# Kernel tuning notes

Measured on AMD Instinct MI355X. Metric: run time of the kernel, lower is better.

## Reference

```python
import jax, jax.numpy as jnp
import numpy as np

B, C, H, W = 4, 256, 128, 128
WS = 16                      # window_size
DA = 64                      # dim_attn = dim // head_dim_reduce_ratio
MID = 1024                   # mid_dim = dim * ratio
SCALE = DA ** -0.5           # num_heads=1 -> dim_head = DA


def setup_inputs() -> dict:
    key = jax.random.key(0)
    ks = jax.random.split(key, 14)
    def w(k, shape, std=0.02):
        return jax.random.normal(k, shape, dtype=jnp.float32) * std
    return {
        "x": jax.random.normal(ks[0], (B, C, H, W), dtype=jnp.float32),
        "q_w": w(ks[1], (DA, C)),
        "q_s": jax.random.uniform(ks[2], (DA,), minval=0.5, maxval=1.5),
        "q_b": w(ks[3], (DA,), 0.1),
        "k_w": w(ks[4], (DA, C)),
        "k_s": jax.random.uniform(ks[5], (DA,), minval=0.5, maxval=1.5),
        "k_b": w(ks[6], (DA,), 0.1),
        "vg_w": w(ks[7], (2 * MID, C)),
        "vg_s": jax.random.uniform(ks[8], (2 * MID,), minval=0.5, maxval=1.5),
        "vg_b": w(ks[9], (2 * MID,), 0.1),
        "p_w": w(ks[10], (C, MID)),
        "p_s": jax.random.uniform(ks[11], (C,), minval=0.5, maxval=1.5),
        "p_b": w(ks[12], (C,), 0.1),
    }


def _conv1x1_bn(xf, w, s, b):
    # xf: [Bw, Cin, N]; 1x1 conv + folded BatchNorm (per-channel affine)
    return jnp.einsum("oc,bcn->bon", w, xf) * s[:, None] + b[:, None]


def reference(x, q_w, q_s, q_b, k_w, k_s, k_b, vg_w, vg_s, vg_b, p_w, p_s, p_b):
    nH, nW = H // WS, W // WS
    # window_partition: [B,C,H,W] -> [B*nH*nW, C, WS, WS]
    xw = x.reshape(B, C, nH, WS, nW, WS).transpose(0, 2, 4, 1, 3, 5)
    xf = xw.reshape(B * nH * nW, C, WS * WS)  # [Bw, C, N]

    # v_gate conv -> sigmoid applied to BOTH halves (matches source)
    vg = jax.nn.sigmoid(_conv1x1_bn(xf, vg_w, vg_s, vg_b))   # [Bw, 2*MID, N]
    v, gate = jnp.split(vg, 2, axis=1)                        # [Bw, MID, N] each

    q = _conv1x1_bn(xf, q_w, q_s, q_b) * SCALE                # [Bw, DA, N]
    k = _conv1x1_bn(xf, k_w, k_s, k_b)                        # [Bw, DA, N]

    attn = jax.nn.softmax(jnp.einsum("bcn,bcm->bnm", q, k), axis=-1)  # [Bw, N, N]
    out = jnp.einsum("bcm,bnm->bcn", v, attn)                 # v @ attn^T -> [Bw, MID, N]
    out = out * gate
    out = _conv1x1_bn(out, p_w, p_s, p_b)                     # [Bw, C, N]

    # window_reverse: [B*nH*nW, C, WS, WS] -> [B, C, H, W]
    out = out.reshape(B, nH, nW, C, WS, WS).transpose(0, 3, 1, 4, 2, 5)
    return out.reshape(B, C, H, W)
```

## Files before the change

### kernel.cpp

```cpp
#include <hip/hip_runtime.h>
#include <hip/hip_bf16.h>

#define B_    4
#define C_    256
#define H_    128
#define W_    128
#define NW_   256
#define N_    256
#define DA_   64
#define MID_  1024
#define SCALE_ 0.125f

typedef __attribute__((ext_vector_type(8))) __bf16 frag8;
typedef __attribute__((ext_vector_type(4))) float  f32x4;
typedef __attribute__((ext_vector_type(4))) unsigned int u32x4;

#define MFMA(a, b, c) __builtin_amdgcn_mfma_f32_16x16x32_bf16(a, b, c, 0, 0, 0)

__device__ __forceinline__ unsigned short f2bf(float x) {
    union { float f; unsigned u; } v; v.f = x;
    unsigned r = v.u + 0x7FFFu + ((v.u >> 16) & 1u);
    return (unsigned short)(r >> 16);
}
__device__ __forceinline__ float bf2f(unsigned short h) {
    union { unsigned u; float f; } v; v.u = ((unsigned)h) << 16;
    return v.f;
}
__device__ __forceinline__ frag8 loadf8(const unsigned short* p) {
    return *reinterpret_cast<const frag8*>(p);
}

__global__ void k_wprep(const float* __restrict__ qw, const float* __restrict__ qs,
                        const float* __restrict__ kw, const float* __restrict__ ks,
                        const float* __restrict__ vgw, const float* __restrict__ vgs,
                        const float* __restrict__ pw, const float* __restrict__ ps,
                        unsigned short* __restrict__ wvg,
                        unsigned short* __restrict__ wqk,
                        unsigned short* __restrict__ wp) {
    int i = blockIdx.x * 256 + threadIdx.x;
    if (i < 2048 * 256) {
        int r = i >> 8;
        wvg[i] = f2bf(vgw[i] * vgs[r]);
        return;
    }
    int j = i - 2048 * 256;
    if (j < 128 * 256) {
        int r = j >> 8, c = j & 255;
        float v = (r < 64) ? qw[r * 256 + c] * qs[r] * SCALE_
                           : kw[(r - 64) * 256 + c] * ks[r - 64];
        wqk[j] = f2bf(v);
        return;
    }
    int m = j - 128 * 256;
    if (m < 256 * 1024) {
        int o = m >> 10;
        wp[m] = f2bf(pw[m] * ps[o]);
    }
}

__global__ void k_pack(const float* __restrict__ x, unsigned short* __restrict__ xfT) {
    __shared__ unsigned short tile[64][258];
    int wdw = blockIdx.x >> 2, cq = blockIdx.x & 3;
    int b = wdw >> 6, wh = (wdw >> 3) & 7, ww = wdw & 7;
    int tid = threadIdx.x;
    int n = tid;
    int h = wh * 16 + (n >> 4), wc = ww * 16 + (n & 15);
    const float* xb = x + ((long)(b * C_ + cq * 64)) * (H_ * W_) + h * W_ + wc;
    #pragma unroll 4
    for (int cl = 0; cl < 64; ++cl)
        tile[cl][n] = f2bf(xb[cl * H_ * W_]);
    __syncthreads();
    unsigned short* dst = xfT + (long)wdw * (N_ * C_) + cq * 64;
    int cl = tid & 63;
    #pragma unroll 4
    for (int it = 0; it < 64; ++it) {
        int nn = it * 4 + (tid >> 6);
        dst[nn * C_ + cl] = tile[cl][nn];
    }
}

__global__ __launch_bounds__(512) void k_attn(const unsigned short* __restrict__ xfT,
                                              const unsigned short* __restrict__ wqk,
                                              const float* __restrict__ qb,
                                              const float* __restrict__ kb,
                                              unsigned short* __restrict__ attn) {
    __shared__ __align__(16) unsigned short qT[256][72];
    __shared__ __align__(16) unsigned short kT[256][72];
    __shared__ __align__(16) char wqlds[65536];
    int wdw = blockIdx.x;
    int tid = threadIdx.x, w = tid >> 6, l = tid & 63;
    int l16 = l & 15, lg = l >> 4;
    const unsigned short* xw = xfT + (long)wdw * (N_ * C_);

    {
        int srow = tid >> 2;
        int cb = (tid & 3) * 128;
        const u32x4* src = reinterpret_cast<const u32x4*>(wqk + srow * 256 + (tid & 3) * 64);
        int sw = (srow & 7) << 4;
        #pragma unroll
        for (int j = 0; j < 8; ++j)
            *reinterpret_cast<u32x4*>(wqlds + srow * 512 + ((cb + j * 16) ^ sw)) = src[j];
    }
    __syncthreads();

    f32x4 acc[8][2];
    #pragma unroll
    for (int a = 0; a < 8; ++a) {
        acc[a][0] = (f32x4){0.f, 0.f, 0.f, 0.f};
        acc[a][1] = (f32x4){0.f, 0.f, 0.f, 0.f};
    }
    for (int kk = 0; kk < 8; ++kk) {
        int c0 = kk * 32 + lg * 8;
        frag8 b0 = loadf8(xw + (32 * w + l16) * 256 + c0);
        frag8 b1 = loadf8(xw + (32 * w + 16 + l16) * 256 + c0);
        int cbyte = c0 * 2;
        #pragma unroll
        for (int rt = 0; rt < 8; ++rt) {
            int row = rt * 16 + l16;
            frag8 af = *reinterpret_cast<const frag8*>(
                wqlds + row * 512 + (cbyte ^ ((row & 7) << 4)));
            acc[rt][0] = MFMA(af, b0, acc[rt][0]);
            acc[rt][1] = MFMA(af, b1, acc[rt][1]);
        }
    }
    #pragma unroll
    for (int rt = 0; rt < 8; ++rt) {
        int rowb = rt * 16 + lg * 4;
        bool isq = rt < 4;
        float b0 = isq ? qb[rowb + 0] * SCALE_ : kb[rowb - 64 + 0];
        float b1 = isq ? qb[rowb + 1] * SCALE_ : kb[rowb - 64 + 1];
        float b2 = isq ? qb[rowb + 2] * SCALE_ : kb[rowb - 64 + 2];
        float b3 = isq ? qb[rowb + 3] * SCALE_ : kb[rowb - 64 + 3];
        #pragma unroll
        for (int ct = 0; ct < 2; ++ct) {
            int col = 32 * w + ct * 16 + l16;
            ushort4 t;
            t.x = f2bf(acc[rt][ct][0] + b0);
            t.y = f2bf(acc[rt][ct][1] + b1);
            t.z = f2bf(acc[rt][ct][2] + b2);
            t.w = f2bf(acc[rt][ct][3] + b3);
            unsigned short* dstp = isq ? &qT[col][rowb] : &kT[col][rowb - 64];
            *reinterpret_cast<ushort4*>(dstp) = t;
        }
    }
    __syncthreads();

    #pragma unroll
    for (int pass = 0; pass < 2; ++pass) {
        int n0 = pass * 128 + w * 16;
        f32x4 a2[16];
        #pragma unroll
        for (int c = 0; c < 16; ++c) a2[c] = (f32x4){0.f, 0.f, 0.f, 0.f};
        #pragma unroll
        for (int kk = 0; kk < 2; ++kk) {
            int k0 = kk * 32 + lg * 8;
            frag8 af = loadf8(&qT[n0 + l16][k0]);
            #pragma unroll
            for (int ct = 0; ct < 16; ++ct) {
                frag8 bf = loadf8(&kT[ct * 16 + l16][k0]);
                a2[ct] = MFMA(af, bf, a2[ct]);
            }
        }
        #pragma unroll
        for (int r = 0; r < 4; ++r) {
            int n = n0 + lg * 4 + r;
            float mx = -1e30f;
            #pragma unroll
            for (int ct = 0; ct < 16; ++ct) mx = fmaxf(mx, a2[ct][r]);
            #pragma unroll
            for (int d = 1; d < 16; d <<= 1) mx = fmaxf(mx, __shfl_xor(mx, d, 64));
            float p[16], s = 0.f;
            #pragma unroll
            for (int ct = 0; ct < 16; ++ct) { p[ct] = __expf(a2[ct][r] - mx); s += p[ct]; }
            #pragma unroll
            for (int d = 1; d < 16; d <<= 1) s += __shfl_xor(s, d, 64);
            float inv = __builtin_amdgcn_rcpf(s);
            unsigned short* dst = attn + (long)wdw * (N_ * N_) + n * 256 + l16;
            #pragma unroll
            for (int ct = 0; ct < 16; ++ct) dst[ct * 16] = f2bf(p[ct] * inv);
        }
    }
}

__device__ __forceinline__ void wstage_load(u32x4 wr[4], const unsigned short* __restrict__ wvg,
                                            int mid0, int h, int tid) {
    int srow = tid >> 2;
    long grow = (srow < 64) ? (long)(mid0 + srow) : (long)(MID_ + mid0 + srow - 64);
    const u32x4* src = reinterpret_cast<const u32x4*>(wvg + grow * 256 + h * 128 + (tid & 3) * 32);
    wr[0] = src[0]; wr[1] = src[1]; wr[2] = src[2]; wr[3] = src[3];
}
__device__ __forceinline__ void wstage_write(const u32x4 wr[4], char* wlds, int tid) {
    int srow = tid >> 2;
    int cb = (tid & 3) * 64;
    int sw = (srow & 7) << 4;
    #pragma unroll
    for (int j = 0; j < 4; ++j)
        *reinterpret_cast<u32x4*>(wlds + srow * 256 + ((cb + j * 16) ^ sw)) = wr[j];
}
__device__ __forceinline__ void vg_mfma_half(const char* wlds,
                                             const unsigned short* __restrict__ xwA,
                                             const unsigned short* __restrict__ xwB,
                                             int h, int l16, int lg, f32x4 accA[8][2]) {
    #pragma unroll
    for (int kkl = 0; kkl < 4; ++kkl) {
        int c0 = h * 128 + kkl * 32 + lg * 8;
        frag8 b0 = loadf8(xwA + c0);
        frag8 b1 = loadf8(xwB + c0);
        int cbase = kkl * 64 + lg * 16;
        #pragma unroll
        for (int rt = 0; rt < 8; ++rt) {
            int row = rt * 16 + l16;
            frag8 af = *reinterpret_cast<const frag8*>(
                wlds + row * 256 + (cbase ^ ((row & 7) << 4)));
            accA[rt][0] = MFMA(af, b0, accA[rt][0]);
            accA[rt][1] = MFMA(af, b1, accA[rt][1]);
        }
    }
}

__global__ __launch_bounds__(512, 4) void k_vgpv(const unsigned short* __restrict__ xfT,
                                                 const unsigned short* __restrict__ attn,
                                                 const unsigned short* __restrict__ wvg,
                                                 const float* __restrict__ vgb,
                                                 unsigned short* __restrict__ pvg) {
    __shared__ __align__(16) unsigned short vlds[64][264];
    __shared__ __align__(16) char wlds[32768];
    __shared__ float vgb_s[256];
    int bid = blockIdx.x;
    int lane8 = bid & 7, rr = bid >> 3;
    int sub = rr & 7, winHi = rr >> 3;
    int wdw = winHi * 8 + lane8;
    int mtbase = sub * 2;

    int tid = threadIdx.x, w = tid >> 6, l = tid & 63;
    int l16 = l & 15, lg = l >> 4;
    int nb = 32 * w;
    const unsigned short* xw = xfT + (long)wdw * (N_ * C_);
    const unsigned short* xwA = xw + (nb + l16) * 256;
    const unsigned short* xwB = xw + (nb + 16 + l16) * 256;
    const unsigned short* aw = attn + (long)wdw * (N_ * N_);
    const unsigned short* awA = aw + (nb + l16) * 256;
    const unsigned short* awB = aw + (nb + 16 + l16) * 256;
    unsigned short* pw_out = pvg + (long)wdw * (N_ * MID_);

    if (tid < 256) {
        int i = tid >> 7, s = tid & 127;
        int src = (s < 64) ? ((mtbase + i) * 64 + s)
                           : (MID_ + (mtbase + i) * 64 + (s - 64));
        vgb_s[tid] = vgb[src];
    }

    int mid0_0 = mtbase * 64, mid0_1 = (mtbase + 1) * 64;
    u32x4 wr[4], wr2[4];
    wstage_load(wr, wvg, mid0_0, 0, tid);
    __syncthreads();

    #pragma unroll
    for (int i = 0; i < 2; ++i) {
        int mid0 = (i == 0) ? mid0_0 : mid0_1;

        f32x4 accA[8][2];
        #pragma unroll
        for (int a = 0; a < 8; ++a) {
            accA[a][0] = (f32x4){0.f, 0.f, 0.f, 0.f};
            accA[a][1] = (f32x4){0.f, 0.f, 0.f, 0.f};
        }

        wstage_write(wr, wlds, tid);
        wstage_load(wr2, wvg, mid0, 1, tid);
        __syncthreads();
        vg_mfma_half(wlds, xwA, xwB, 0, l16, lg, accA);
        __syncthreads();

        wstage_write(wr2, wlds, tid);
        if (i == 0) wstage_load(wr, wvg, mid0_1, 0, tid);
        __syncthreads();
        vg_mfma_half(wlds, xwA, xwB, 1, l16, lg, accA);

        unsigned gpack[4][2][2];
        #pragma unroll
        for (int rt = 0; rt < 8; ++rt) {
            #pragma unroll
            for (int ct = 0; ct < 2; ++ct) {
                int col = nb + ct * 16 + l16;
                unsigned short sgb[4];
                #pragma unroll
                for (int r = 0; r < 4; ++r) {
                    int s = rt * 16 + lg * 4 + r;
                    float bias = vgb_s[i * 128 + s];
                    float t = accA[rt][ct][r] + bias;
                    sgb[r] = f2bf(__builtin_amdgcn_rcpf(1.f + __expf(-t)));
                }
                if (rt < 4) {
                    #pragma unroll
                    for (int r = 0; r < 4; ++r)
                        vlds[rt * 16 + lg * 4 + r][col] = sgb[r];
                } else {
                    gpack[rt - 4][ct][0] = (unsigned)sgb[0] | ((unsigned)sgb[1] << 16);
                    gpack[rt - 4][ct][1] = (unsigned)sgb[2] | ((unsigned)sgb[3] << 16);
                }
            }
        }
        __syncthreads();

        f32x4 acc2[4][2];
        #pragma unroll
        for (int a = 0; a < 4; ++a) {
            acc2[a][0] = (f32x4){0.f, 0.f, 0.f, 0.f};
            acc2[a][1] = (f32x4){0.f, 0.f, 0.f, 0.f};
        }
        #pragma unroll 2
        for (int kk = 0; kk < 8; ++kk) {
            int m0 = kk * 32 + lg * 8;
            frag8 b0 = loadf8(awA + m0);
            frag8 b1 = loadf8(awB + m0);
            #pragma unroll
            for (int rt = 0; rt < 4; ++rt) {
                frag8 av = loadf8(&vlds[rt * 16 + l16][m0]);
                acc2[rt][0] = MFMA(av, b0, acc2[rt][0]);
                acc2[rt][1] = MFMA(av, b1, acc2[rt][1]);
            }
        }
        __syncthreads();

        #pragma unroll
        for (int rt = 0; rt < 4; ++rt) {
            int midb = mid0 + rt * 16 + lg * 4;
            #pragma unroll
            for (int ct = 0; ct < 2; ++ct) {
                int n = nb + ct * 16 + l16;
                unsigned g01 = gpack[rt][ct][0], g23 = gpack[rt][ct][1];
                ushort4 t;
                t.x = f2bf(acc2[rt][ct][0] * bf2f((unsigned short)(g01 & 0xffff)));
                t.y = f2bf(acc2[rt][ct][1] * bf2f((unsigned short)(g01 >> 16)));
                t.z = f2bf(acc2[rt][ct][2] * bf2f((unsigned short)(g23 & 0xffff)));
                t.w = f2bf(acc2[rt][ct][3] * bf2f((unsigned short)(g23 >> 16)));
                *reinterpret_cast<ushort4*>(pw_out + (long)n * MID_ + midb) = t;
            }
        }
    }
}

__global__ __launch_bounds__(256, 4) void k_pconv(const unsigned short* __restrict__ pvg,
                                                  const unsigned short* __restrict__ wp,
                                                  const float* __restrict__ pb,
                                                  float* __restrict__ out) {
    __shared__ __align__(16) char wplds[32768];
    __shared__ float pbs[256];
    int bid = blockIdx.x;
    int win = bid >> 2, q = bid & 3;
    int tid = threadIdx.x, w = tid >> 6, l = tid & 63;
    int l16 = l & 15, lg = l >> 4;
    int nbase = q * 64 + w * 16;
    const unsigned short* bp = pvg + ((long)win * N_ + nbase) * MID_;
    const unsigned short* wrow = wp + (long)tid * MID_;

    pbs[tid] = pb[tid];

    f32x4 acc[16];
    #pragma unroll
    for (int c = 0; c < 16; ++c) acc[c] = (f32x4){0.f, 0.f, 0.f, 0.f};

    u32x4 wr[8];
    #pragma unroll
    for (int j = 0; j < 8; ++j)
        wr[j] = *reinterpret_cast<const u32x4*>(wrow + j * 8);
    __syncthreads();

    int sw = (tid & 7) << 4;
    for (int c = 0; c < 16; ++c) {
        #pragma unroll
        for (int j = 0; j < 8; ++j)
            *reinterpret_cast<u32x4*>(wplds + tid * 128 + ((j * 16) ^ sw)) = wr[j];
        __syncthreads();
        if (c < 15) {
            #pragma unroll
            for (int j = 0; j < 8; ++j)
                wr[j] = *reinterpret_cast<const u32x4*>(wrow + (c + 1) * 64 + j * 8);
        }
        #pragma unroll
        for (int kk2 = 0; kk2 < 2; ++kk2) {
            int k0 = c * 64 + kk2 * 32 + lg * 8;
            frag8 bf = loadf8(bp + l16 * MID_ + k0);
            int slot = (kk2 * 4 + lg) * 16;
            #pragma unroll
            for (int ct = 0; ct < 16; ++ct) {
                int row = ct * 16 + l16;
                frag8 af = *reinterpret_cast<const frag8*>(
                    wplds + row * 128 + (slot ^ ((row & 7) << 4)));
                acc[ct] = MFMA(af, bf, acc[ct]);
            }
        }
        __syncthreads();
    }

    int b = win >> 6, wh = (win >> 3) & 7, ww = win & 7;
    int h = wh * 16 + q * 4 + w;
    int wc = ww * 16 + l16;
    #pragma unroll
    for (int ct = 0; ct < 16; ++ct) {
        #pragma unroll
        for (int r = 0; r < 4; ++r) {
            int cc = ct * 16 + lg * 4 + r;
            out[((long)(b * C_ + cc)) * (H_ * W_) + h * W_ + wc] = acc[ct][r] + pbs[cc];
        }
    }
}

__global__ __launch_bounds__(512, 2) void k_main(const unsigned short* __restrict__ xfT,
                                                 const unsigned short* __restrict__ attn,
                                                 const unsigned short* __restrict__ wvg,
                                                 const unsigned short* __restrict__ wp,
                                                 const float* __restrict__ vgb,
                                                 const float* __restrict__ pb,
                                                 float* __restrict__ out) {
    __shared__ __align__(16) unsigned short vlds[64][264];
    __shared__ __align__(16) unsigned short glds[64][264];
    __shared__ __align__(16) unsigned short pvgT[256][72];
    __shared__ float vgb_s[2048];
    __shared__ float pb_s[256];
    int wdw = blockIdx.x;
    int tid = threadIdx.x, w = tid >> 6, l = tid & 63;
    int l16 = l & 15, lg = l >> 4;
    int nb = 32 * w;
    const unsigned short* xw = xfT + (long)wdw * (N_ * C_);
    const unsigned short* aw = attn + (long)wdw * (N_ * N_);

    {
        float4 v = reinterpret_cast<const float4*>(vgb)[tid];
        reinterpret_cast<float4*>(vgb_s)[tid] = v;
        if (tid < 256) pb_s[tid] = pb[tid];
    }

    f32x4 acc3[16][2];
    #pragma unroll
    for (int a = 0; a < 16; ++a)
        #pragma unroll
        for (int c = 0; c < 2; ++c) acc3[a][c] = (f32x4){0.f, 0.f, 0.f, 0.f};

    __syncthreads();

    for (int mt = 0; mt < 16; ++mt) {
        int mid0 = mt * 64;
        f32x4 accA[8][2];
        #pragma unroll
        for (int a = 0; a < 8; ++a) {
            accA[a][0] = (f32x4){0.f, 0.f, 0.f, 0.f};
            accA[a][1] = (f32x4){0.f, 0.f, 0.f, 0.f};
        }
        for (int kk = 0; kk < 8; ++kk) {
            int c0 = kk * 32 + lg * 8;
            frag8 b0 = loadf8(xw + (nb + l16) * 256 + c0);
            frag8 b1 = loadf8(xw + (nb + 16 + l16) * 256 + c0);
            #pragma unroll
            for (int rt = 0; rt < 8; ++rt) {
                int s = rt * 16 + l16;
                int row = (rt < 4) ? (mid0 + s) : (MID_ + mid0 + s - 64);
                frag8 af = loadf8(wvg + row * 256 + c0);
                accA[rt][0] = MFMA(af, b0, accA[rt][0]);
                accA[rt][1] = MFMA(af, b1, accA[rt][1]);
            }
        }
        #pragma unroll
        for (int rt = 0; rt < 8; ++rt) {
            #pragma unroll
            for (int ct = 0; ct < 2; ++ct) {
                int col = nb + ct * 16 + l16;
                #pragma unroll
                for (int r = 0; r < 4; ++r) {
                    int s = rt * 16 + lg * 4 + r;
                    float bias = (rt < 4) ? vgb_s[mid0 + s] : vgb_s[MID_ + mid0 + s - 64];
                    float t = accA[rt][ct][r] + bias;
                    float sg = __builtin_amdgcn_rcpf(1.f + __expf(-t));
                    if (rt < 4) vlds[s][col] = f2bf(sg);
                    else        glds[s - 64][col] = f2bf(sg);
                }
            }
        }
        __syncthreads();

        f32x4 acc2[4][2];
        #pragma unroll
        for (int a = 0; a < 4; ++a) {
            acc2[a][0] = (f32x4){0.f, 0.f, 0.f, 0.f};
            acc2[a][1] = (f32x4){0.f, 0.f, 0.f, 0.f};
        }
        for (int kk = 0; kk < 8; ++kk) {
            int m0 = kk * 32 + lg * 8;
            frag8 b0 = loadf8(aw + (nb + l16) * 256 + m0);
            frag8 b1 = loadf8(aw + (nb + 16 + l16) * 256 + m0);
            #pragma unroll
            for (int rt = 0; rt < 4; ++rt) {
                frag8 av = loadf8(&vlds[rt * 16 + l16][m0]);
                acc2[rt][0] = MFMA(av, b0, acc2[rt][0]);
                acc2[rt][1] = MFMA(av, b1, acc2[rt][1]);
            }
        }
        {
            #pragma unroll
            for (int rt = 0; rt < 4; ++rt) {
                int midb = rt * 16 + lg * 4;
                #pragma unroll
                for (int ct = 0; ct < 2; ++ct) {
                    int n = nb + ct * 16 + l16;
                    ushort4 t;
                    t.x = f2bf(acc2[rt][ct][0] * bf2f(glds[midb + 0][n]));
                    t.y = f2bf(acc2[rt][ct][1] * bf2f(glds[midb + 1][n]));
                    t.z = f2bf(acc2[rt][ct][2] * bf2f(glds[midb + 2][n]));
                    t.w = f2bf(acc2[rt][ct][3] * bf2f(glds[midb + 3][n]));
                    *reinterpret_cast<ushort4*>(&pvgT[n][midb]) = t;
                }
            }
        }
        __syncthreads();

        #pragma unroll
        for (int kk2 = 0; kk2 < 2; ++kk2) {
            int k0 = kk2 * 32 + lg * 8;
            frag8 b0 = loadf8(&pvgT[nb + l16][k0]);
            frag8 b1 = loadf8(&pvgT[nb + 16 + l16][k0]);
            #pragma unroll
            for (int rt = 0; rt < 16; ++rt) {
                frag8 ap = loadf8(wp + (rt * 16 + l16) * 1024 + mid0 + k0);
                acc3[rt][0] = MFMA(ap, b0, acc3[rt][0]);
                acc3[rt][1] = MFMA(ap, b1, acc3[rt][1]);
            }
        }
    }

    int b = wdw >> 6, wh = (wdw >> 3) & 7, ww = wdw & 7;
    #pragma unroll
    for (int rt = 0; rt < 16; ++rt) {
        #pragma unroll
        for (int ct = 0; ct < 2; ++ct) {
            int h = wh * 16 + 2 * w + ct;
            int wc = ww * 16 + l16;
            #pragma unroll
            for (int r = 0; r < 4; ++r) {
                int c = rt * 16 + lg * 4 + r;
                out[(((long)(b * C_ + c)) * H_ + h) * W_ + wc] = acc3[rt][ct][r] + pb_s[c];
            }
        }
    }
}

extern "C" void kernel_launch(void* const* d_in, const int* in_sizes, int n_in,
                              void* d_out, int out_size, void* d_ws, size_t ws_size,
                              hipStream_t stream) {
    const float* x    = (const float*)d_in[0];
    const float* q_w  = (const float*)d_in[1];
    const float* q_s  = (const float*)d_in[2];
    const float* q_b  = (const float*)d_in[3];
    const float* k_w  = (const float*)d_in[4];
    const float* k_s  = (const float*)d_in[5];
    const float* k_b  = (const float*)d_in[6];
    const float* vg_w = (const float*)d_in[7];
    const float* vg_s = (const float*)d_in[8];
    const float* vg_b = (const float*)d_in[9];
    const float* p_w  = (const float*)d_in[10];
    const float* p_s  = (const float*)d_in[11];
    const float* p_b  = (const float*)d_in[12];

    unsigned short* xfT  = (unsigned short*)d_ws;
    unsigned short* attn = xfT + (size_t)NW_ * N_ * C_;
    unsigned short* wvg  = attn + (size_t)NW_ * N_ * N_;
    unsigned short* wqk  = wvg + 2048 * 256;
    unsigned short* wp   = wqk + 128 * 256;
    unsigned short* pvg  = wp + 256 * 1024;
    size_t base_elems = (size_t)NW_ * N_ * C_ + (size_t)NW_ * N_ * N_ +
                        2048 * 256 + 128 * 256 + 256 * 1024;
    size_t need_fused = base_elems * sizeof(unsigned short);
    size_t need_split = (base_elems + (size_t)NW_ * N_ * MID_) * sizeof(unsigned short);
    if (ws_size < need_fused) return;

    k_wprep<<<3200, 256, 0, stream>>>(q_w, q_s, k_w, k_s, vg_w, vg_s, p_w, p_s,
                                      wvg, wqk, wp);
    k_pack<<<1024, 256, 0, stream>>>(x, xfT);
    k_attn<<<NW_, 512, 0, stream>>>(xfT, wqk, q_b, k_b, attn);
    if (ws_size >= need_split) {
        k_vgpv<<<NW_ * 8, 512, 0, stream>>>(xfT, attn, wvg, vg_b, pvg);
        k_pconv<<<NW_ * 4, 256, 0, stream>>>(pvg, wp, p_b, (float*)d_out);
    } else {
        k_main<<<NW_, 512, 0, stream>>>(xfT, attn, wvg, wp, vg_b, p_b, (float*)d_out);
    }
}
```

Before: 364.9 us.

## Shrink k_vgpv LDS footprint with quarter-K weight staging and swizzled V buffer

```diff
diff --git a/kernel.cpp b/kernel.cpp
--- a/kernel.cpp
+++ b/kernel.cpp
@@ -182,28 +182,28 @@
     }
 }
 
-__device__ __forceinline__ void wstage_load(u32x4 wr[4], const unsigned short* __restrict__ wvg,
-                                            int mid0, int h, int tid) {
+__device__ __forceinline__ void wstage_load_q(u32x4 wr[2], const unsigned short* __restrict__ wvg,
+                                              int mid0, int q, int tid) {
     int srow = tid >> 2;
     long grow = (srow < 64) ? (long)(mid0 + srow) : (long)(MID_ + mid0 + srow - 64);
-    const u32x4* src = reinterpret_cast<const u32x4*>(wvg + grow * 256 + h * 128 + (tid & 3) * 32);
-    wr[0] = src[0]; wr[1] = src[1]; wr[2] = src[2]; wr[3] = src[3];
-}
-__device__ __forceinline__ void wstage_write(const u32x4 wr[4], char* wlds, int tid) {
+    const u32x4* src = reinterpret_cast<const u32x4*>(wvg + grow * 256 + q * 64 + (tid & 3) * 16);
+    wr[0] = src[0];
+    wr[1] = src[1];
+}
+__device__ __forceinline__ void wstage_write_q(const u32x4 wr[2], char* wlds, int tid) {
     int srow = tid >> 2;
-    int cb = (tid & 3) * 64;
+    int cb = (tid & 3) * 32;
     int sw = (srow & 7) << 4;
-    #pragma unroll
-    for (int j = 0; j < 4; ++j)
-        *reinterpret_cast<u32x4*>(wlds + srow * 256 + ((cb + j * 16) ^ sw)) = wr[j];
-}
-__device__ __forceinline__ void vg_mfma_half(const char* wlds,
-                                             const unsigned short* __restrict__ xwA,
-                                             const unsigned short* __restrict__ xwB,
-                                             int h, int l16, int lg, f32x4 accA[8][2]) {
-    #pragma unroll
-    for (int kkl = 0; kkl < 4; ++kkl) {
-        int c0 = h * 128 + kkl * 32 + lg * 8;
+    *reinterpret_cast<u32x4*>(wlds + srow * 128 + (cb ^ sw)) = wr[0];
+    *reinterpret_cast<u32x4*>(wlds + srow * 128 + ((cb + 16) ^ sw)) = wr[1];
+}
+__device__ __forceinline__ void vg_mfma_q(const char* wlds,
+                                          const unsigned short* __restrict__ xwA,
+                                          const unsigned short* __restrict__ xwB,
+                                          int q, int l16, int lg, f32x4 accA[8][2]) {
+    #pragma unroll
+    for (int kkl = 0; kkl < 2; ++kkl) {
+        int c0 = q * 64 + kkl * 32 + lg * 8;
         frag8 b0 = loadf8(xwA + c0);
         frag8 b1 = loadf8(xwB + c0);
         int cbase = kkl * 64 + lg * 16;
@@ -211,20 +211,20 @@
         for (int rt = 0; rt < 8; ++rt) {
             int row = rt * 16 + l16;
             frag8 af = *reinterpret_cast<const frag8*>(
-                wlds + row * 256 + (cbase ^ ((row & 7) << 4)));
+                wlds + row * 128 + (cbase ^ ((row & 7) << 4)));
             accA[rt][0] = MFMA(af, b0, accA[rt][0]);
             accA[rt][1] = MFMA(af, b1, accA[rt][1]);
         }
     }
 }
 
-__global__ __launch_bounds__(512, 4) void k_vgpv(const unsigned short* __restrict__ xfT,
+__global__ __launch_bounds__(512, 6) void k_vgpv(const unsigned short* __restrict__ xfT,
                                                  const unsigned short* __restrict__ attn,
                                                  const unsigned short* __restrict__ wvg,
                                                  const float* __restrict__ vgb,
                                                  unsigned short* __restrict__ pvg) {
-    __shared__ __align__(16) unsigned short vlds[64][264];
-    __shared__ __align__(16) char wlds[32768];
+    __shared__ __align__(16) char vldsb[32768];
+    __shared__ __align__(16) char wlds[16384];
     __shared__ float vgb_s[256];
     int bid = blockIdx.x;
     int lane8 = bid & 7, rr = bid >> 3;
@@ -251,8 +251,8 @@
     }
 
     int mid0_0 = mtbase * 64, mid0_1 = (mtbase + 1) * 64;
-    u32x4 wr[4], wr2[4];
-    wstage_load(wr, wvg, mid0_0, 0, tid);
+    u32x4 wr[2], wrn[2];
+    wstage_load_q(wr, wvg, mid0_0, 0, tid);
     __syncthreads();
 
     #pragma unroll
@@ -266,16 +266,16 @@
             accA[a][1] = (f32x4){0.f, 0.f, 0.f, 0.f};
         }
 
-        wstage_write(wr, wlds, tid);
-        wstage_load(wr2, wvg, mid0, 1, tid);
-        __syncthreads();
-        vg_mfma_half(wlds, xwA, xwB, 0, l16, lg, accA);
-        __syncthreads();
-
-        wstage_write(wr2, wlds, tid);
-        if (i == 0) wstage_load(wr, wvg, mid0_1, 0, tid);
-        __syncthreads();
-        vg_mfma_half(wlds, xwA, xwB, 1, l16, lg, accA);
+        #pragma unroll
+        for (int q = 0; q < 4; ++q) {
+            wstage_write_q(wr, wlds, tid);
+            if (q < 3)          wstage_load_q(wrn, wvg, mid0, q + 1, tid);
+            else if (i == 0)    wstage_load_q(wrn, wvg, mid0_1, 0, tid);
+            __syncthreads();
+            vg_mfma_q(wlds, xwA, xwB, q, l16, lg, accA);
+            __syncthreads();
+            wr[0] = wrn[0]; wr[1] = wrn[1];
+        }
 
         unsigned gpack[4][2][2];
         #pragma unroll
@@ -293,8 +293,11 @@
                 }
                 if (rt < 4) {
                     #pragma unroll
-                    for (int r = 0; r < 4; ++r)
-                        vlds[rt * 16 + lg * 4 + r][col] = sgb[r];
+                    for (int r = 0; r < 4; ++r) {
+                        int s = rt * 16 + lg * 4 + r;
+                        *reinterpret_cast<unsigned short*>(
+                            vldsb + s * 512 + ((col * 2) ^ ((s & 7) << 4))) = sgb[r];
+                    }
                 } else {
                     gpack[rt - 4][ct][0] = (unsigned)sgb[0] | ((unsigned)sgb[1] << 16);
                     gpack[rt - 4][ct][1] = (unsigned)sgb[2] | ((unsigned)sgb[3] << 16);
@@ -316,7 +319,9 @@
             frag8 b1 = loadf8(awB + m0);
             #pragma unroll
             for (int rt = 0; rt < 4; ++rt) {
-                frag8 av = loadf8(&vlds[rt * 16 + l16][m0]);
+                int row = rt * 16 + l16;
+                frag8 av = *reinterpret_cast<const frag8*>(
+                    vldsb + row * 512 + ((m0 * 2) ^ ((row & 7) << 4)));
                 acc2[rt][0] = MFMA(av, b0, acc2[rt][0]);
                 acc2[rt][1] = MFMA(av, b1, acc2[rt][1]);
             }
```

New measurement: 956.7 us. +162.2%, slower.
